# Performance work log

Hardware: AMD Instinct MI355X
Metric: run time of the kernel (lower is better)

## Reference

```python
import jax, jax.numpy as jnp
import numpy as np

B, S, E = 8, 1024, 512      # batch, seq, emb_size
L, H, K, F = 2, 4, 4, 128    # blocks, heads, conv kernel, final_size
I = 2 * E                    # inner dim (proj_factor=2)
DH = I // H                  # head dim
EPS = 1e-5


def _layernorm(x, g, b):
    mu = jnp.mean(x, axis=-1, keepdims=True)
    var = jnp.var(x, axis=-1, keepdims=True)
    return (x - mu) * jax.lax.rsqrt(var + EPS) * g + b


def _causal_conv(x, w, b):
    # x: [B,S,I], w: [K,I] depthwise, left-padded causal conv
    y = jax.lax.conv_general_dilated(
        x, w[:, None, :], window_strides=(1,), padding=[(K - 1, 0)],
        dimension_numbers=('NWC', 'WIO', 'NWC'), feature_group_count=I)
    return y + b


def _mlstm_parallel(q, k, v, ipre, fpre):
    # q,k,v: [B,H,S,DH]; ipre,fpre: [B,H,S]  (stabilized parallel mLSTM)
    lf = jax.nn.log_sigmoid(fpre)                       # [B,H,S]
    lfc = jnp.cumsum(lf, axis=-1)
    logD = lfc[..., :, None] - lfc[..., None, :] + ipre[..., None, :]  # [B,H,S,S]
    mask = jnp.tril(jnp.ones((S, S), dtype=bool))
    logD = jnp.where(mask, logD, -jnp.inf)
    m = jnp.max(logD, axis=-1, keepdims=True)           # [B,H,S,1]
    Dm = jnp.exp(logD - m)
    scores = jnp.einsum('bhtd,bhsd->bhts', q, k) * (DH ** -0.5) * Dm
    n = jnp.maximum(jnp.abs(jnp.sum(scores, axis=-1, keepdims=True)), jnp.exp(-m))
    return jnp.einsum('bhts,bhsd->bhtd', scores, v) / n


def _block(x, ln_g, ln_b, w_up, conv_w, conv_b, wq, wk, wv,
           w_i, b_i, w_f, b_f, skip, gn_g, w_down, b_down):
    res = x
    xn = _layernorm(x, ln_g, ln_b)
    up = xn @ w_up                                      # [B,S,2I]
    x_m, z = up[..., :I], up[..., I:]
    c_act = jax.nn.silu(_causal_conv(x_m, conv_w, conv_b))
    q = c_act @ wq
    k = c_act @ wk
    v = x_m @ wv
    qkv = jnp.concatenate([q, k, v], axis=-1)           # [B,S,3I]
    ipre = jnp.transpose(qkv @ w_i + b_i, (0, 2, 1))    # [B,H,S]
    fpre = jnp.transpose(qkv @ w_f + b_f, (0, 2, 1))
    to_h = lambda t: jnp.transpose(t.reshape(B, S, H, DH), (0, 2, 1, 3))
    h = _mlstm_parallel(to_h(q), to_h(k), to_h(v), ipre, fpre)  # [B,H,S,DH]
    # per-head group norm
    mu = jnp.mean(h, axis=-1, keepdims=True)
    var = jnp.var(h, axis=-1, keepdims=True)
    h = (h - mu) * jax.lax.rsqrt(var + EPS)
    h = jnp.transpose(h, (0, 2, 1, 3)).reshape(B, S, I) * gn_g
    h = h + skip * c_act
    h = h * jax.nn.silu(z)
    return res + h @ w_down + b_down


def setup_inputs() -> dict:
    key = jax.random.key(0)
    ks = jax.random.split(key, 12)
    n = lambda k, shp, s=0.02: jax.random.normal(k, shp, jnp.float32) * s
    return {
        'x': jax.random.normal(ks[0], (B, S, E), jnp.float32),
        'ln_g': jnp.ones((L, E), jnp.float32), 'ln_b': jnp.zeros((L, E), jnp.float32),
        'w_up': n(ks[1], (L, E, 2 * I)),
        'conv_w': n(ks[2], (L, K, I), 0.1), 'conv_b': jnp.zeros((L, I), jnp.float32),
        'wq': n(ks[3], (L, I, I)), 'wk': n(ks[4], (L, I, I)), 'wv': n(ks[5], (L, I, I)),
        'w_i': n(ks[6], (L, 3 * I, H)), 'b_i': jnp.zeros((L, H), jnp.float32),
        'w_f': n(ks[7], (L, 3 * I, H)), 'b_f': 3.0 * jnp.ones((L, H), jnp.float32),
        'skip': jnp.ones((L, I), jnp.float32), 'gn_g': jnp.ones((L, I), jnp.float32),
        'w_down': n(ks[8], (L, I, E)), 'b_down': jnp.zeros((L, E), jnp.float32),
        'w_fin': n(ks[9], (E, F)), 'b_fin': jnp.zeros((F,), jnp.float32),
    }


def reference(x, ln_g, ln_b, w_up, conv_w, conv_b, wq, wk, wv, w_i, b_i,
              w_f, b_f, skip, gn_g, w_down, b_down, w_fin, b_fin):
    h = x
    for l in range(L):  # 2 structurally identical mLSTM blocks
        h = _block(h, ln_g[l], ln_b[l], w_up[l], conv_w[l], conv_b[l],
                   wq[l], wk[l], wv[l], w_i[l], b_i[l], w_f[l], b_f[l],
                   skip[l], gn_g[l], w_down[l], b_down[l])
    return h @ w_fin + b_fin
```

## Files before the change

kernel.cpp:

```cpp
#include <hip/hip_runtime.h>
#include <math.h>

#define S_LEN 1024
#define I_DIM 1024
#define DH_   256
#define H_NUM 4
#define B_NUM 8
#define ROWS  (B_NUM*S_LEN)

#define GLOBAL_AS __attribute__((address_space(1)))
#define LDS_AS    __attribute__((address_space(3)))

#define VM0    asm volatile("s_waitcnt vmcnt(0)" ::: "memory")
#define LGKM0  asm volatile("s_waitcnt lgkmcnt(0)" ::: "memory")
#define BAR    __builtin_amdgcn_s_barrier()
#define SFENCE __builtin_amdgcn_sched_barrier(0)

typedef __attribute__((ext_vector_type(8))) short bf16x8;
typedef __attribute__((ext_vector_type(4))) float f32x4;
typedef unsigned short u16;

__device__ __forceinline__ u16 f2bf(float f) {
    union { float f; unsigned u; } v; v.f = f;
    unsigned r = v.u + 0x7FFF + ((v.u >> 16) & 1);
    return (u16)(r >> 16);
}
__device__ __forceinline__ float bf2f(u16 h) {
    union { unsigned u; float f; } v; v.u = ((unsigned)h) << 16;
    return v.f;
}

__global__ __launch_bounds__(64) void ln_fused_k(const float* __restrict__ x,
                                                 const float* __restrict__ g,
                                                 const float* __restrict__ b,
                                                 u16* __restrict__ out) {
    int row = blockIdx.x, lane = threadIdx.x;
    const float* xr = x + (size_t)row * 512;
    float4 a = *(const float4*)&xr[lane * 8];
    float4 c = *(const float4*)&xr[lane * 8 + 4];
    float s  = a.x + a.y + a.z + a.w + c.x + c.y + c.z + c.w;
    float s2 = a.x*a.x + a.y*a.y + a.z*a.z + a.w*a.w
             + c.x*c.x + c.y*c.y + c.z*c.z + c.w*c.w;
#pragma unroll
    for (int off = 32; off > 0; off >>= 1) {
        s  += __shfl_down(s, off);
        s2 += __shfl_down(s2, off);
    }
    s = __shfl(s, 0); s2 = __shfl(s2, 0);
    float mu = s * (1.f / 512.f);
    float rstd = rsqrtf(s2 * (1.f / 512.f) - mu * mu + 1e-5f);
    int e0 = lane * 8;
    float y[8] = {a.x,a.y,a.z,a.w,c.x,c.y,c.z,c.w};
    ushort4 o0, o1;
    o0.x = f2bf((y[0]-mu)*rstd*g[e0+0]+b[e0+0]);
    o0.y = f2bf((y[1]-mu)*rstd*g[e0+1]+b[e0+1]);
    o0.z = f2bf((y[2]-mu)*rstd*g[e0+2]+b[e0+2]);
    o0.w = f2bf((y[3]-mu)*rstd*g[e0+3]+b[e0+3]);
    o1.x = f2bf((y[4]-mu)*rstd*g[e0+4]+b[e0+4]);
    o1.y = f2bf((y[5]-mu)*rstd*g[e0+5]+b[e0+5]);
    o1.z = f2bf((y[6]-mu)*rstd*g[e0+6]+b[e0+6]);
    o1.w = f2bf((y[7]-mu)*rstd*g[e0+7]+b[e0+7]);
    *(ushort4*)&out[(size_t)row * 512 + e0]     = o0;
    *(ushort4*)&out[(size_t)row * 512 + e0 + 4] = o1;
}

__global__ __launch_bounds__(256) void cvtT_k(const float* __restrict__ W,
                                              u16* __restrict__ Wt, int K, int N) {
    __shared__ float t[32][33];
    int k0 = blockIdx.x * 32, n0 = blockIdx.y * 32;
    int c = threadIdx.x & 31, r8 = threadIdx.x >> 5;
#pragma unroll
    for (int q = 0; q < 4; q++) {
        int r = r8 * 4 + q;
        t[r][c] = W[(size_t)(k0 + r) * N + n0 + c];
    }
    __syncthreads();
#pragma unroll
    for (int q = 0; q < 4; q++) {
        int r = r8 * 4 + q;
        Wt[(size_t)(n0 + r) * K + k0 + c] = f2bf(t[c][r]);
    }
}

__global__ __launch_bounds__(256) void vt_k(const u16* __restrict__ v,
                                            u16* __restrict__ vt) {
    __shared__ u16 t[32][34];
    int s0 = blockIdx.x * 32, d0 = blockIdx.y * 32, bh = blockIdx.z;
    int b = bh >> 2, h = bh & 3;
    int c = threadIdx.x & 31, r4 = threadIdx.x >> 5;
#pragma unroll
    for (int q = 0; q < 4; q++) {
        int r = r4 * 4 + q;
        t[r][c] = v[(size_t)(b * 1024 + s0 + r) * I_DIM + h * 256 + d0 + c];
    }
    __syncthreads();
#pragma unroll
    for (int q = 0; q < 4; q++) {
        int r = r4 * 4 + q;
        vt[((size_t)bh * 256 + d0 + r) * 1024 + s0 + c] = t[c][r];
    }
}

template<int EPI>
__global__ __launch_bounds__(256) void gemm_bf16_k(
    const u16* __restrict__ A, const u16* __restrict__ Wt, int N, int K,
    float* __restrict__ Cf, u16* __restrict__ Cb,
    const float* __restrict__ bias, const float* __restrict__ res, int ldres)
{
    __shared__ __align__(16) u16 As[2][128 * 32];
    __shared__ __align__(16) u16 Bs[2][128 * 32];
    int tid = threadIdx.x;
    int lane = tid & 63;
    int wm = (tid >> 6) & 1, wn = tid >> 7;
    int gx = gridDim.x;
    int nwg = gx * gridDim.y;
    int bid = blockIdx.y * gx + blockIdx.x;
    int cpx = nwg >> 3;
    int swz = (bid & 7) * cpx + (bid >> 3);
    int r0 = (swz / gx) * 128, n0 = (swz % gx) * 128;

    int arow = tid >> 2, acol = (tid & 3) * 8;
    const u16* ap0 = A  + (size_t)(r0 + arow) * K + acol;
    const u16* ap1 = A  + (size_t)(r0 + 64 + arow) * K + acol;
    const u16* bp0 = Wt + (size_t)(n0 + arow) * K + acol;
    const u16* bp1 = Wt + (size_t)(n0 + 64 + arow) * K + acol;

    auto stage = [&](int kt, int bs) {
        int koff = kt * 32;
        __builtin_amdgcn_global_load_lds((const GLOBAL_AS unsigned int*)(ap0 + koff), (LDS_AS unsigned int*)&As[bs][tid * 8], 16, 0, 0);
        __builtin_amdgcn_global_load_lds((const GLOBAL_AS unsigned int*)(ap1 + koff), (LDS_AS unsigned int*)&As[bs][2048 + tid * 8], 16, 0, 0);
        __builtin_amdgcn_global_load_lds((const GLOBAL_AS unsigned int*)(bp0 + koff), (LDS_AS unsigned int*)&Bs[bs][tid * 8], 16, 0, 0);
        __builtin_amdgcn_global_load_lds((const GLOBAL_AS unsigned int*)(bp1 + koff), (LDS_AS unsigned int*)&Bs[bs][2048 + tid * 8], 16, 0, 0);
    };

    f32x4 acc[4][4];
#pragma unroll
    for (int i = 0; i < 4; i++)
#pragma unroll
        for (int j = 0; j < 4; j++) acc[i][j] = (f32x4){0.f, 0.f, 0.f, 0.f};

    int lm = lane & 15, lk = (lane >> 4) * 8;
    int nt = K >> 5;
    stage(0, 0);
    VM0; BAR; SFENCE;
    for (int t = 0; t < nt; ++t) {
        int cur = t & 1;
        if (t + 1 < nt) stage(t + 1, cur ^ 1);
        bf16x8 af[4], bfr[4];
#pragma unroll
        for (int f = 0; f < 4; f++) {
            af[f]  = *(const bf16x8*)&As[cur][(wm * 64 + f * 16 + lm) * 32 + lk];
            bfr[f] = *(const bf16x8*)&Bs[cur][(wn * 64 + f * 16 + lm) * 32 + lk];
        }
#pragma unroll
        for (int i = 0; i < 4; i++)
#pragma unroll
            for (int j = 0; j < 4; j++)
                acc[i][j] = __builtin_amdgcn_mfma_f32_16x16x32_bf16(af[i], bfr[j], acc[i][j], 0, 0, 0);
        VM0; BAR; SFENCE;
    }
    int lr = (lane >> 4) * 4;
#pragma unroll
    for (int i = 0; i < 4; i++) {
#pragma unroll
        for (int j = 0; j < 4; j++) {
#pragma unroll
            for (int q = 0; q < 4; q++) {
                int row = r0 + wm * 64 + i * 16 + lr + q;
                int col = n0 + wn * 64 + j * 16 + lm;
                float o = acc[i][j][q];
                if (EPI == 0) {
                    Cb[(size_t)row * N + col] = f2bf(o);
                } else if (EPI == 1) {
                    if (col < 1024) Cb[(size_t)row * 1024 + col] = f2bf(o);
                    else            Cf[(size_t)row * 1024 + (col - 1024)] = o;
                } else if (EPI == 2) {
                    o += bias[col] + res[(size_t)row * ldres + col];
                    Cf[(size_t)row * N + col] = o;
                    Cb[(size_t)row * N + col] = f2bf(o);
                } else {
                    o += bias[col];
                    Cf[(size_t)row * N + col] = o;
                }
            }
        }
    }
}

__global__ __launch_bounds__(256) void conv_k(const u16* __restrict__ xm,
                                              const float* __restrict__ w,
                                              const float* __restrict__ cb,
                                              u16* __restrict__ cact) {
    int idx = blockIdx.x * 256 + threadIdx.x;
    int r = idx >> 8;
    int c = (idx & 255) * 4;
    int t = r & 1023;
    const u16* base = xm + (size_t)(r - t) * I_DIM;
    float4 acc = *(const float4*)&cb[c];
#pragma unroll
    for (int j = 0; j < 4; j++) {
        int tt = t - 3 + j;
        if (tt >= 0) {
            short4 s = *(const short4*)&base[(size_t)tt * I_DIM + c];
            float4 wv = *(const float4*)&w[j * I_DIM + c];
            acc.x = fmaf(bf2f((u16)s.x), wv.x, acc.x);
            acc.y = fmaf(bf2f((u16)s.y), wv.y, acc.y);
            acc.z = fmaf(bf2f((u16)s.z), wv.z, acc.z);
            acc.w = fmaf(bf2f((u16)s.w), wv.w, acc.w);
        }
    }
    acc.x = acc.x / (1.f + __expf(-acc.x));
    acc.y = acc.y / (1.f + __expf(-acc.y));
    acc.z = acc.z / (1.f + __expf(-acc.z));
    acc.w = acc.w / (1.f + __expf(-acc.w));
    ushort4 o;
    o.x = f2bf(acc.x); o.y = f2bf(acc.y); o.z = f2bf(acc.z); o.w = f2bf(acc.w);
    *(ushort4*)&cact[(size_t)r * I_DIM + c] = o;
}

__global__ __launch_bounds__(256) void gates_k(const u16* __restrict__ qk,
                                               const u16* __restrict__ v,
                                               const float* __restrict__ wi,
                                               const float* __restrict__ bi,
                                               const float* __restrict__ wf,
                                               const float* __restrict__ bf,
                                               float* __restrict__ ipre,
                                               float* __restrict__ fpre) {
    int r0 = blockIdx.x * 4;
    int tid = threadIdx.x;
    float ai[4][4], af4[4][4];
#pragma unroll
    for (int r = 0; r < 4; r++)
#pragma unroll
        for (int m = 0; m < 4; m++) { ai[r][m] = 0.f; af4[r][m] = 0.f; }
#pragma unroll
    for (int part = 0; part < 3; part++) {
        const u16* src; size_t st;
        if (part == 0)      { src = qk + (size_t)r0 * 2048;        st = 2048; }
        else if (part == 1) { src = qk + (size_t)r0 * 2048 + 1024; st = 2048; }
        else                { src = v  + (size_t)r0 * 1024;        st = 1024; }
        const float* wip = wi + part * I_DIM * 4;
        const float* wfp = wf + part * I_DIM * 4;
#pragma unroll
        for (int jj = 0; jj < 4; jj++) {
            int e = tid + jj * 256;
            float4 w4  = *(const float4*)&wip[e * 4];
            float4 f4v = *(const float4*)&wfp[e * 4];
#pragma unroll
            for (int r = 0; r < 4; r++) {
                float xv = bf2f(src[(size_t)r * st + e]);
                ai[r][0] = fmaf(xv, w4.x, ai[r][0]);
                ai[r][1] = fmaf(xv, w4.y, ai[r][1]);
                ai[r][2] = fmaf(xv, w4.z, ai[r][2]);
                ai[r][3] = fmaf(xv, w4.w, ai[r][3]);
                af4[r][0] = fmaf(xv, f4v.x, af4[r][0]);
                af4[r][1] = fmaf(xv, f4v.y, af4[r][1]);
                af4[r][2] = fmaf(xv, f4v.z, af4[r][2]);
                af4[r][3] = fmaf(xv, f4v.w, af4[r][3]);
            }
        }
    }
#pragma unroll
    for (int off = 32; off > 0; off >>= 1) {
#pragma unroll
        for (int r = 0; r < 4; r++)
#pragma unroll
            for (int m = 0; m < 4; m++) {
                ai[r][m]  += __shfl_down(ai[r][m], off);
                af4[r][m] += __shfl_down(af4[r][m], off);
            }
    }
    __shared__ float red[4][32];
    int wv_ = tid >> 6, lane = tid & 63;
    if (lane == 0) {
#pragma unroll
        for (int r = 0; r < 4; r++)
#pragma unroll
            for (int m = 0; m < 4; m++) {
                red[wv_][r * 8 + m]     = ai[r][m];
                red[wv_][r * 8 + 4 + m] = af4[r][m];
            }
    }
    __syncthreads();
    if (tid < 32) {
        int r = tid >> 3, m = tid & 7;
        float s_ = red[0][tid] + red[1][tid] + red[2][tid] + red[3][tid];
        int row = r0 + r, bb = row >> 10, ss = row & 1023;
        if (m < 4) ipre[((size_t)(bb * 4 + m)) * 1024 + ss] = s_ + bi[m];
        else       fpre[((size_t)(bb * 4 + (m - 4))) * 1024 + ss] = s_ + bf[m - 4];
    }
}

__global__ __launch_bounds__(1024) void scan_k(const float* __restrict__ ipre,
                                               const float* __restrict__ fpre,
                                               float* __restrict__ cA,
                                               float* __restrict__ MA,
                                               float* __restrict__ nF) {
    __shared__ float buf[1024];
    int bh = blockIdx.x, t = threadIdx.x;
    size_t base = (size_t)bh * 1024;
    float fp = fpre[base + t];
    float lf = (fp >= 0.f) ? -log1pf(expf(-fp)) : (fp - log1pf(expf(fp)));
    buf[t] = lf; __syncthreads();
    for (int off = 1; off < 1024; off <<= 1) {
        float u = (t >= off) ? buf[t - off] : 0.f;
        __syncthreads();
        buf[t] += u;
        __syncthreads();
    }
    float lfc = buf[t];
    float c = ipre[base + t] - lfc;
    __syncthreads();
    buf[t] = c; __syncthreads();
    for (int off = 1; off < 1024; off <<= 1) {
        float u = (t >= off) ? buf[t - off] : -3.4e38f;
        __syncthreads();
        buf[t] = fmaxf(buf[t], u);
        __syncthreads();
    }
    float M = buf[t];
    cA[base + t] = c * 1.44269504f;
    MA[base + t] = M * 1.44269504f;
    nF[base + t] = expf(-(lfc + M));
}

__global__ __launch_bounds__(256) void attn_k(
    const u16* __restrict__ qg, const u16* __restrict__ kg, const u16* __restrict__ vt,
    const float* __restrict__ c2A, const float* __restrict__ M2A, const float* __restrict__ nFl,
    const u16* __restrict__ cact, const float* __restrict__ zb, u16* __restrict__ hb,
    const float* __restrict__ gng, const float* __restrict__ skip)
{
    __shared__ __align__(16) u16 Kb[2][32 * 256];
    __shared__ __align__(16) u16 Ps[32 * 40];
    __shared__ float rs2[4][16];
    __shared__ float rsI[32];
    __shared__ float gS[32 * 4];
    __shared__ float gQ[32 * 4];
    __shared__ float gmu[32], gvr[32];

    int tid = threadIdx.x;
    int w = tid >> 6, l = tid & 63;
    int lm = l & 15, lk = l >> 4;
    int i0 = blockIdx.x;
    int g = (i0 & 7) * 128 + (i0 >> 3);
    int b = g >> 7, h = (g >> 5) & 3, bx = g & 31;
    int T0 = (31 - bx) * 32;
    int tf = w & 1, sf = w >> 1;
    int bh32 = b * H_NUM + h;
    size_t bh = (size_t)bh32 * S_LEN;

    bf16x8 qf[8];
    {
        size_t base = ((size_t)(b * S_LEN + T0 + tf * 16 + lm)) * 2048 + h * DH_ + lk * 8;
#pragma unroll
        for (int ks = 0; ks < 8; ks++) qf[ks] = *(const bf16x8*)&qg[base + ks * 32];
    }
    f32x4 acc[2][4];
#pragma unroll
    for (int i = 0; i < 2; i++)
#pragma unroll
        for (int jd = 0; jd < 4; jd++) acc[i][jd] = (f32x4){0.f, 0.f, 0.f, 0.f};
    float rsum[4] = {0, 0, 0, 0};
    float m2r[4]; int tg[4];
#pragma unroll
    for (int q = 0; q < 4; q++) {
        tg[q] = T0 + tf * 16 + lk * 4 + q;
        m2r[q] = M2A[bh + tg[q]];
    }

    const size_t krow0 = (size_t)(b * S_LEN) * 2048 + h * DH_;
    const u16* vptr = vt + (size_t)bh32 * 256 * S_LEN + (size_t)(w * 64 + lm) * S_LEN + lk * 8;

    auto stageK = [&](int s0, int bs) {
#pragma unroll
        for (int r = 0; r < 4; r++) {
            int q = r * 256 + tid;
            int row = q >> 5, cl = q & 31;
            int cs = cl ^ (row & 7);
            const u16* src = kg + krow0 + (size_t)(s0 + row) * 2048 + cs * 8;
            __builtin_amdgcn_global_load_lds((const GLOBAL_AS unsigned int*)src,
                                             (LDS_AS unsigned int*)&Kb[bs][q * 8], 16, 0, 0);
        }
    };

    int nst = (T0 >> 5) + 1;
    stageK(0, 0);
    bf16x8 vA[4], vB[4];
    float c2c, c2n;
#pragma unroll
    for (int jd = 0; jd < 4; jd++) vA[jd] = *(const bf16x8*)(vptr + jd * 16 * S_LEN);
    c2c = c2A[bh + sf * 16 + lm];
    VM0; BAR; SFENCE;

    for (int st = 0; st < nst; st++) {
        int s0 = st * 32;
        int cur = st & 1;
        int more = (st + 1 < nst);
        if (more) {
            stageK(s0 + 32, cur ^ 1);
#pragma unroll
            for (int jd = 0; jd < 4; jd++) vB[jd] = *(const bf16x8*)(vptr + jd * 16 * S_LEN + s0 + 32);
            c2n = c2A[bh + s0 + 32 + sf * 16 + lm];
        }
        f32x4 sacc = (f32x4){0.f, 0.f, 0.f, 0.f};
        __builtin_amdgcn_s_setprio(1);
#pragma unroll
        for (int ks = 0; ks < 8; ks++) {
            int row = sf * 16 + lm;
            int ch = (ks * 4 + lk) ^ (row & 7);
            bf16x8 kf = *(const bf16x8*)&Kb[cur][row * 256 + ch * 8];
            sacc = __builtin_amdgcn_mfma_f32_16x16x32_bf16(qf[ks], kf, sacc, 0, 0, 0);
        }
        __builtin_amdgcn_s_setprio(0);
        {
            int sg = s0 + sf * 16 + lm;
#pragma unroll
            for (int q = 0; q < 4; q++) {
                float v = sacc[q] * 0.0625f * __builtin_amdgcn_exp2f(c2c - m2r[q]);
                v = (sg <= tg[q]) ? v : 0.f;
                u16 pb = f2bf(v);
                rsum[q] += bf2f(pb);
                Ps[(tf * 16 + lk * 4 + q) * 40 + sf * 16 + lm] = pb;
            }
        }
        LGKM0; BAR; SFENCE;
        __builtin_amdgcn_s_setprio(1);
#pragma unroll
        for (int i = 0; i < 2; i++) {
            bf16x8 pa = *(const bf16x8*)&Ps[(i * 16 + lm) * 40 + lk * 8];
#pragma unroll
            for (int jd = 0; jd < 4; jd++)
                acc[i][jd] = __builtin_amdgcn_mfma_f32_16x16x32_bf16(pa, vA[jd], acc[i][jd], 0, 0, 0);
        }
        __builtin_amdgcn_s_setprio(0);
        VM0; BAR; SFENCE;
        if (more) {
#pragma unroll
            for (int jd = 0; jd < 4; jd++) vA[jd] = vB[jd];
            c2c = c2n;
        }
    }
    {
#pragma unroll
        for (int m = 1; m < 16; m <<= 1) {
#pragma unroll
            for (int q = 0; q < 4; q++) rsum[q] += __shfl_xor(rsum[q], m);
        }
        if (lm == 0) {
#pragma unroll
            for (int q = 0; q < 4; q++) rs2[w][lk * 4 + q] = rsum[q];
        }
    }
    __syncthreads();
    if (tid < 32) {
        int tfi = tid >> 4, idx = tid & 15;
        float s = rs2[tfi][idx] + rs2[tfi + 2][idx];
        float n = fmaxf(fabsf(s), nFl[bh + T0 + tid]);
        rsI[tid] = 1.f / n;
    }
    __syncthreads();
#pragma unroll
    for (int i = 0; i < 2; i++) {
#pragma unroll
        for (int q = 0; q < 4; q++) {
            int rl = i * 16 + lk * 4 + q;
            float inv = rsI[rl];
            float ps = 0.f, pq = 0.f;
#pragma unroll
            for (int jd = 0; jd < 4; jd++) {
                float v = acc[i][jd][q] * inv;
                acc[i][jd][q] = v;
                ps += v; pq += v * v;
            }
#pragma unroll
            for (int m = 1; m < 16; m <<= 1) {
                ps += __shfl_xor(ps, m);
                pq += __shfl_xor(pq, m);
            }
            if (lm == 0) { gS[rl * 4 + w] = ps; gQ[rl * 4 + w] = pq; }
        }
    }
    __syncthreads();
    if (tid < 32) {
        float s1 = gS[tid*4] + gS[tid*4+1] + gS[tid*4+2] + gS[tid*4+3];
        float s2 = gQ[tid*4] + gQ[tid*4+1] + gQ[tid*4+2] + gQ[tid*4+3];
        float mu = s1 * (1.f / 256.f);
        float var = s2 * (1.f / 256.f) - mu * mu;
        gmu[tid] = mu;
        gvr[tid] = rsqrtf(var + 1e-5f);
    }
    __syncthreads();
#pragma unroll
    for (int i = 0; i < 2; i++) {
#pragma unroll
        for (int q = 0; q < 4; q++) {
            int rl = i * 16 + lk * 4 + q;
            size_t r = (size_t)b * S_LEN + T0 + rl;
            float mu = gmu[rl], rv = gvr[rl];
#pragma unroll
            for (int jd = 0; jd < 4; jd++) {
                int cix = h * DH_ + w * 64 + jd * 16 + lm;
                float val = (acc[i][jd][q] - mu) * rv * gng[cix];
                float ca = bf2f(cact[r * I_DIM + cix]);
                float z = zb[r * I_DIM + cix];
                float hm = (val + skip[cix] * ca) * (z / (1.f + __expf(-z)));
                hb[r * I_DIM + cix] = f2bf(hm);
            }
        }
    }
}

extern "C" void kernel_launch(void* const* d_in, const int* in_sizes, int n_in,
                              void* d_out, int out_size, void* d_ws, size_t ws_size,
                              hipStream_t stream) {
    const float* x      = (const float*)d_in[0];
    const float* ln_g   = (const float*)d_in[1];
    const float* ln_b   = (const float*)d_in[2];
    const float* w_up   = (const float*)d_in[3];
    const float* conv_w = (const float*)d_in[4];
    const float* conv_b = (const float*)d_in[5];
    const float* wq     = (const float*)d_in[6];
    const float* wk     = (const float*)d_in[7];
    const float* wv     = (const float*)d_in[8];
    const float* w_i    = (const float*)d_in[9];
    const float* b_i    = (const float*)d_in[10];
    const float* w_f    = (const float*)d_in[11];
    const float* b_f    = (const float*)d_in[12];
    const float* skip   = (const float*)d_in[13];
    const float* gn_g   = (const float*)d_in[14];
    const float* w_down = (const float*)d_in[15];
    const float* b_down = (const float*)d_in[16];
    const float* w_fin  = (const float*)d_in[17];
    const float* b_fin  = (const float*)d_in[18];

    char* p = (char*)d_ws;
    auto alloc = [&](size_t bytes) { void* r = p; p += (bytes + 255) & ~(size_t)255; return r; };
    float* zbuf  = (float*)alloc((size_t)ROWS * 1024 * 4);
    float* xa    = (float*)alloc((size_t)ROWS * 512 * 4);
    float* xb2   = (float*)alloc((size_t)ROWS * 512 * 4);
    u16*  xln    = (u16*)alloc((size_t)ROWS * 512 * 2);
    u16*  xm     = (u16*)alloc((size_t)ROWS * 1024 * 2);
    u16*  cactb  = (u16*)alloc((size_t)ROWS * 1024 * 2);
    u16*  qkbf   = (u16*)alloc((size_t)ROWS * 2048 * 2);
    u16*  vbf    = (u16*)alloc((size_t)ROWS * 1024 * 2);
    u16*  vtg    = (u16*)alloc((size_t)32 * 256 * 1024 * 2);
    u16*  hbf    = (u16*)alloc((size_t)ROWS * 1024 * 2);
    u16*  xoutb  = (u16*)alloc((size_t)ROWS * 512 * 2);
    u16*  wupT   = (u16*)alloc((size_t)2 * 2048 * 512 * 2);
    u16*  wqkT   = (u16*)alloc((size_t)2 * 2048 * 1024 * 2);
    u16*  wvT    = (u16*)alloc((size_t)2 * 1024 * 1024 * 2);
    u16*  wdT    = (u16*)alloc((size_t)2 * 512 * 1024 * 2);
    u16*  wfT    = (u16*)alloc((size_t)128 * 512 * 2);
    float* ipre  = (float*)alloc(32768 * 4);
    float* fpre  = (float*)alloc(32768 * 4);
    float* cA    = (float*)alloc(32768 * 4);
    float* MA    = (float*)alloc(32768 * 4);
    float* nF    = (float*)alloc(32768 * 4);

    for (int l = 0; l < 2; l++) {
        cvtT_k<<<dim3(16, 64), 256, 0, stream>>>(w_up + (size_t)l * 512 * 2048, wupT + (size_t)l * 2048 * 512, 512, 2048);
        cvtT_k<<<dim3(32, 32), 256, 0, stream>>>(wq + (size_t)l * 1024 * 1024, wqkT + (size_t)l * 2048 * 1024, 1024, 1024);
        cvtT_k<<<dim3(32, 32), 256, 0, stream>>>(wk + (size_t)l * 1024 * 1024, wqkT + (size_t)l * 2048 * 1024 + 1024 * 1024, 1024, 1024);
        cvtT_k<<<dim3(32, 32), 256, 0, stream>>>(wv + (size_t)l * 1024 * 1024, wvT + (size_t)l * 1024 * 1024, 1024, 1024);
        cvtT_k<<<dim3(32, 16), 256, 0, stream>>>(w_down + (size_t)l * 1024 * 512, wdT + (size_t)l * 512 * 1024, 1024, 512);
    }
    cvtT_k<<<dim3(16, 4), 256, 0, stream>>>(w_fin, wfT, 512, 128);

    const float* xin = x;
    for (int l = 0; l < 2; l++) {
        float* xout = (l == 0) ? xa : xb2;
        ln_fused_k<<<ROWS, 64, 0, stream>>>(xin, ln_g + l * 512, ln_b + l * 512, xln);
        gemm_bf16_k<1><<<dim3(16, 64), 256, 0, stream>>>(
            xln, wupT + (size_t)l * 2048 * 512, 2048, 512, zbuf, xm, nullptr, nullptr, 0);
        conv_k<<<ROWS, 256, 0, stream>>>(xm, conv_w + l * 4 * I_DIM, conv_b + l * I_DIM, cactb);
        gemm_bf16_k<0><<<dim3(8, 64), 256, 0, stream>>>(
            xm, wvT + (size_t)l * 1024 * 1024, 1024, 1024, nullptr, vbf, nullptr, nullptr, 0);
        gemm_bf16_k<0><<<dim3(16, 64), 256, 0, stream>>>(
            cactb, wqkT + (size_t)l * 2048 * 1024, 2048, 1024, nullptr, qkbf, nullptr, nullptr, 0);
        vt_k<<<dim3(32, 8, 32), 256, 0, stream>>>(vbf, vtg);
        gates_k<<<ROWS / 4, 256, 0, stream>>>(qkbf, vbf,
            w_i + l * 3072 * 4, b_i + l * 4, w_f + l * 3072 * 4, b_f + l * 4, ipre, fpre);
        scan_k<<<32, 1024, 0, stream>>>(ipre, fpre, cA, MA, nF);
        attn_k<<<dim3(1024), 256, 0, stream>>>(qkbf, qkbf + 1024, vtg, cA, MA, nF, cactb, zbuf, hbf,
            gn_g + l * I_DIM, skip + l * I_DIM);
        gemm_bf16_k<2><<<dim3(4, 64), 256, 0, stream>>>(
            hbf, wdT + (size_t)l * 512 * 1024, 512, 1024, xout, xoutb,
            b_down + l * 512, xin, 512);
        xin = xout;
    }
    gemm_bf16_k<3><<<dim3(1, 64), 256, 0, stream>>>(
        xoutb, wfT, 128, 512, (float*)d_out, nullptr, b_fin, nullptr, 0);
}
```

Baseline: 714.9 us.

## Software-pipeline attention loop so QK of step t overlaps PV of step t-1

Restructures the causal attention loop so the score MFMAs for the current K tile run alongside the PV MFMAs for the previous tile. The P tile is double-buffered in LDS, and the per-iteration barrier count drops from two to one, removing the explicit vmcnt wait. V fragments are now loaded one step later, into a staging register set. The gain is fewer barriers and more independent MFMA work per iteration. The risk is that the asynchronous LDS K loads are no longer guaranteed complete before the barrier, which depends on how the compiler places the vmcnt wait.

```diff
diff --git a/kernel.cpp b/kernel.cpp
--- a/kernel.cpp
+++ b/kernel.cpp
@@ -331,7 +331,7 @@
     const float* __restrict__ gng, const float* __restrict__ skip)
 {
     __shared__ __align__(16) u16 Kb[2][32 * 256];
-    __shared__ __align__(16) u16 Ps[32 * 40];
+    __shared__ __align__(16) u16 Ps[2][32 * 40];
     __shared__ float rs2[4][16];
     __shared__ float rsI[32];
     __shared__ float gS[32 * 4];
@@ -387,32 +387,30 @@
     stageK(0, 0);
     bf16x8 vA[4], vB[4];
     float c2c, c2n;
-#pragma unroll
-    for (int jd = 0; jd < 4; jd++) vA[jd] = *(const bf16x8*)(vptr + jd * 16 * S_LEN);
     c2c = c2A[bh + sf * 16 + lm];
     VM0; BAR; SFENCE;
 
-    for (int st = 0; st < nst; st++) {
-        int s0 = st * 32;
-        int cur = st & 1;
-        int more = (st + 1 < nst);
-        if (more) {
-            stageK(s0 + 32, cur ^ 1);
-#pragma unroll
-            for (int jd = 0; jd < 4; jd++) vB[jd] = *(const bf16x8*)(vptr + jd * 16 * S_LEN + s0 + 32);
-            c2n = c2A[bh + s0 + 32 + sf * 16 + lm];
-        }
-        f32x4 sacc = (f32x4){0.f, 0.f, 0.f, 0.f};
-        __builtin_amdgcn_s_setprio(1);
-#pragma unroll
-        for (int ks = 0; ks < 8; ks++) {
-            int row = sf * 16 + lm;
-            int ch = (ks * 4 + lk) ^ (row & 7);
-            bf16x8 kf = *(const bf16x8*)&Kb[cur][row * 256 + ch * 8];
-            sacc = __builtin_amdgcn_mfma_f32_16x16x32_bf16(qf[ks], kf, sacc, 0, 0, 0);
-        }
-        __builtin_amdgcn_s_setprio(0);
-        {
+    for (int t = 0; t <= nst; t++) {
+        int s0 = t * 32;
+        int kc = t & 1;
+        bool qp = (t < nst);
+        bool more = (t + 1 < nst);
+        if (qp) {
+            if (more) stageK(s0 + 32, kc ^ 1);
+            SFENCE;
+#pragma unroll
+            for (int jd = 0; jd < 4; jd++) vB[jd] = *(const bf16x8*)(vptr + jd * 16 * S_LEN + s0);
+            if (more) c2n = c2A[bh + s0 + 32 + sf * 16 + lm];
+            f32x4 sacc = (f32x4){0.f, 0.f, 0.f, 0.f};
+            __builtin_amdgcn_s_setprio(1);
+#pragma unroll
+            for (int ks = 0; ks < 8; ks++) {
+                int row = sf * 16 + lm;
+                int ch = (ks * 4 + lk) ^ (row & 7);
+                bf16x8 kf = *(const bf16x8*)&Kb[kc][row * 256 + ch * 8];
+                sacc = __builtin_amdgcn_mfma_f32_16x16x32_bf16(qf[ks], kf, sacc, 0, 0, 0);
+            }
+            __builtin_amdgcn_s_setprio(0);
             int sg = s0 + sf * 16 + lm;
 #pragma unroll
             for (int q = 0; q < 4; q++) {
@@ -420,25 +418,26 @@
                 v = (sg <= tg[q]) ? v : 0.f;
                 u16 pb = f2bf(v);
                 rsum[q] += bf2f(pb);
-                Ps[(tf * 16 + lk * 4 + q) * 40 + sf * 16 + lm] = pb;
-            }
+                Ps[kc][(tf * 16 + lk * 4 + q) * 40 + sf * 16 + lm] = pb;
+            }
+        }
+        if (t > 0) {
+            __builtin_amdgcn_s_setprio(1);
+#pragma unroll
+            for (int i = 0; i < 2; i++) {
+                bf16x8 pa = *(const bf16x8*)&Ps[kc ^ 1][(i * 16 + lm) * 40 + lk * 8];
+#pragma unroll
+                for (int jd = 0; jd < 4; jd++)
+                    acc[i][jd] = __builtin_amdgcn_mfma_f32_16x16x32_bf16(pa, vA[jd], acc[i][jd], 0, 0, 0);
+            }
+            __builtin_amdgcn_s_setprio(0);
+        }
+        if (qp) {
+#pragma unroll
+            for (int jd = 0; jd < 4; jd++) vA[jd] = vB[jd];
+            if (more) c2c = c2n;
         }
         LGKM0; BAR; SFENCE;
-        __builtin_amdgcn_s_setprio(1);
-#pragma unroll
-        for (int i = 0; i < 2; i++) {
-            bf16x8 pa = *(const bf16x8*)&Ps[(i * 16 + lm) * 40 + lk * 8];
-#pragma unroll
-            for (int jd = 0; jd < 4; jd++)
-                acc[i][jd] = __builtin_amdgcn_mfma_f32_16x16x32_bf16(pa, vA[jd], acc[i][jd], 0, 0, 0);
-        }
-        __builtin_amdgcn_s_setprio(0);
-        VM0; BAR; SFENCE;
-        if (more) {
-#pragma unroll
-            for (int jd = 0; jd < 4; jd++) vA[jd] = vB[jd];
-            c2c = c2n;
-        }
     }
     {
 #pragma unroll
```

Measured after the change: 712.3 us. About the same (-0.4%).

## Give each wave its own 16-row query tile in mLSTM attention, dropping LDS staging

Applied to the files above, without the earlier changes.

Restructures the attention kernel so each wave independently owns a 16-row query tile over the full 256-wide head dimension. K and V fragments are now loaded straight from global memory instead of being staged cooperatively into double-buffered LDS. Block-wide barriers are gone, and the normalisation and group-norm reductions now happen within a wave via shuffles. The grid is halved and the launch bound now requests 3 blocks per CU. In exchange, K/V reuse across waves through LDS is lost, there is no prefetch overlap, and register pressure rises from 16 accumulator tiles per wave.

```diff
diff --git a/kernel.cpp b/kernel.cpp
--- a/kernel.cpp
+++ b/kernel.cpp
@@ -324,188 +324,127 @@
     nF[base + t] = expf(-(lfc + M));
 }
 
-__global__ __launch_bounds__(256) void attn_k(
+__global__ __launch_bounds__(256, 3) void attn_k(
     const u16* __restrict__ qg, const u16* __restrict__ kg, const u16* __restrict__ vt,
     const float* __restrict__ c2A, const float* __restrict__ M2A, const float* __restrict__ nFl,
     const u16* __restrict__ cact, const float* __restrict__ zb, u16* __restrict__ hb,
     const float* __restrict__ gng, const float* __restrict__ skip)
 {
-    __shared__ __align__(16) u16 Kb[2][32 * 256];
-    __shared__ __align__(16) u16 Ps[32 * 40];
-    __shared__ float rs2[4][16];
-    __shared__ float rsI[32];
-    __shared__ float gS[32 * 4];
-    __shared__ float gQ[32 * 4];
-    __shared__ float gmu[32], gvr[32];
+    __shared__ __align__(16) u16 Ps[4][16 * 40];
 
     int tid = threadIdx.x;
     int w = tid >> 6, l = tid & 63;
     int lm = l & 15, lk = l >> 4;
-    int i0 = blockIdx.x;
-    int g = (i0 & 7) * 128 + (i0 >> 3);
-    int b = g >> 7, h = (g >> 5) & 3, bx = g & 31;
-    int T0 = (31 - bx) * 32;
-    int tf = w & 1, sf = w >> 1;
+    int bid = blockIdx.x;
+    int g = (bid & 7) * 64 + (bid >> 3);
+    int b = g >> 6, rr = g & 63;
+    int h = rr >> 4, tb = rr & 15;
+    int tt = tb * 4 + w;
+    int T0w = (63 - tt) * 16;
+    int nst = (T0w >> 5) + 1;
     int bh32 = b * H_NUM + h;
     size_t bh = (size_t)bh32 * S_LEN;
 
     bf16x8 qf[8];
     {
-        size_t base = ((size_t)(b * S_LEN + T0 + tf * 16 + lm)) * 2048 + h * DH_ + lk * 8;
-#pragma unroll
-        for (int ks = 0; ks < 8; ks++) qf[ks] = *(const bf16x8*)&qg[base + ks * 32];
-    }
-    f32x4 acc[2][4];
-#pragma unroll
-    for (int i = 0; i < 2; i++)
-#pragma unroll
-        for (int jd = 0; jd < 4; jd++) acc[i][jd] = (f32x4){0.f, 0.f, 0.f, 0.f};
+        size_t qbase = ((size_t)(b * S_LEN + T0w + lm)) * 2048 + h * DH_ + lk * 8;
+#pragma unroll
+        for (int ks = 0; ks < 8; ks++) qf[ks] = *(const bf16x8*)&qg[qbase + ks * 32];
+    }
+    f32x4 acc[16];
+#pragma unroll
+    for (int jd = 0; jd < 16; jd++) acc[jd] = (f32x4){0.f, 0.f, 0.f, 0.f};
     float rsum[4] = {0, 0, 0, 0};
     float m2r[4]; int tg[4];
 #pragma unroll
     for (int q = 0; q < 4; q++) {
-        tg[q] = T0 + tf * 16 + lk * 4 + q;
+        tg[q] = T0w + lk * 4 + q;
         m2r[q] = M2A[bh + tg[q]];
     }
 
-    const size_t krow0 = (size_t)(b * S_LEN) * 2048 + h * DH_;
-    const u16* vptr = vt + (size_t)bh32 * 256 * S_LEN + (size_t)(w * 64 + lm) * S_LEN + lk * 8;
-
-    auto stageK = [&](int s0, int bs) {
-#pragma unroll
-        for (int r = 0; r < 4; r++) {
-            int q = r * 256 + tid;
-            int row = q >> 5, cl = q & 31;
-            int cs = cl ^ (row & 7);
-            const u16* src = kg + krow0 + (size_t)(s0 + row) * 2048 + cs * 8;
-            __builtin_amdgcn_global_load_lds((const GLOBAL_AS unsigned int*)src,
-                                             (LDS_AS unsigned int*)&Kb[bs][q * 8], 16, 0, 0);
-        }
-    };
-
-    int nst = (T0 >> 5) + 1;
-    stageK(0, 0);
-    bf16x8 vA[4], vB[4];
-    float c2c, c2n;
-#pragma unroll
-    for (int jd = 0; jd < 4; jd++) vA[jd] = *(const bf16x8*)(vptr + jd * 16 * S_LEN);
-    c2c = c2A[bh + sf * 16 + lm];
-    VM0; BAR; SFENCE;
+    const u16* kp0 = kg + (size_t)(b * S_LEN + lm) * 2048 + h * DH_ + lk * 8;
+    const u16* kp1 = kp0 + 16 * 2048;
+    const u16* vp  = vt + ((size_t)bh32 * 256 + lm) * S_LEN + lk * 8;
+    u16* Pw = Ps[w];
 
     for (int st = 0; st < nst; st++) {
         int s0 = st * 32;
-        int cur = st & 1;
-        int more = (st + 1 < nst);
-        if (more) {
-            stageK(s0 + 32, cur ^ 1);
-#pragma unroll
-            for (int jd = 0; jd < 4; jd++) vB[jd] = *(const bf16x8*)(vptr + jd * 16 * S_LEN + s0 + 32);
-            c2n = c2A[bh + s0 + 32 + sf * 16 + lm];
-        }
-        f32x4 sacc = (f32x4){0.f, 0.f, 0.f, 0.f};
-        __builtin_amdgcn_s_setprio(1);
+        float c2x0 = c2A[bh + s0 + lm];
+        float c2x1 = c2A[bh + s0 + 16 + lm];
+        f32x4 sa0 = (f32x4){0.f,0.f,0.f,0.f};
+        f32x4 sa1 = (f32x4){0.f,0.f,0.f,0.f};
+        const u16* k0p = kp0 + (size_t)s0 * 2048;
+        const u16* k1p = kp1 + (size_t)s0 * 2048;
 #pragma unroll
         for (int ks = 0; ks < 8; ks++) {
-            int row = sf * 16 + lm;
-            int ch = (ks * 4 + lk) ^ (row & 7);
-            bf16x8 kf = *(const bf16x8*)&Kb[cur][row * 256 + ch * 8];
-            sacc = __builtin_amdgcn_mfma_f32_16x16x32_bf16(qf[ks], kf, sacc, 0, 0, 0);
-        }
-        __builtin_amdgcn_s_setprio(0);
-        {
-            int sg = s0 + sf * 16 + lm;
+            bf16x8 k0 = *(const bf16x8*)(k0p + ks * 32);
+            bf16x8 k1 = *(const bf16x8*)(k1p + ks * 32);
+            sa0 = __builtin_amdgcn_mfma_f32_16x16x32_bf16(qf[ks], k0, sa0, 0, 0, 0);
+            sa1 = __builtin_amdgcn_mfma_f32_16x16x32_bf16(qf[ks], k1, sa1, 0, 0, 0);
+        }
+#pragma unroll
+        for (int js = 0; js < 2; js++) {
+            int sg = s0 + js * 16 + lm;
+            float c2 = js ? c2x1 : c2x0;
 #pragma unroll
             for (int q = 0; q < 4; q++) {
-                float v = sacc[q] * 0.0625f * __builtin_amdgcn_exp2f(c2c - m2r[q]);
+                float v = (js ? sa1[q] : sa0[q]) * 0.0625f * __builtin_amdgcn_exp2f(c2 - m2r[q]);
                 v = (sg <= tg[q]) ? v : 0.f;
                 u16 pb = f2bf(v);
                 rsum[q] += bf2f(pb);
-                Ps[(tf * 16 + lk * 4 + q) * 40 + sf * 16 + lm] = pb;
+                Pw[(lk * 4 + q) * 40 + js * 16 + lm] = pb;
             }
         }
-        LGKM0; BAR; SFENCE;
-        __builtin_amdgcn_s_setprio(1);
-#pragma unroll
-        for (int i = 0; i < 2; i++) {
-            bf16x8 pa = *(const bf16x8*)&Ps[(i * 16 + lm) * 40 + lk * 8];
-#pragma unroll
-            for (int jd = 0; jd < 4; jd++)
-                acc[i][jd] = __builtin_amdgcn_mfma_f32_16x16x32_bf16(pa, vA[jd], acc[i][jd], 0, 0, 0);
-        }
-        __builtin_amdgcn_s_setprio(0);
-        VM0; BAR; SFENCE;
-        if (more) {
-#pragma unroll
-            for (int jd = 0; jd < 4; jd++) vA[jd] = vB[jd];
-            c2c = c2n;
-        }
-    }
-    {
+        SFENCE; LGKM0; SFENCE;
+        bf16x8 pa = *(const bf16x8*)&Pw[lm * 40 + lk * 8];
+        const u16* vsp = vp + s0;
+#pragma unroll
+        for (int jd = 0; jd < 16; jd++) {
+            bf16x8 vf = *(const bf16x8*)(vsp + (size_t)jd * 16 * S_LEN);
+            acc[jd] = __builtin_amdgcn_mfma_f32_16x16x32_bf16(pa, vf, acc[jd], 0, 0, 0);
+        }
+        SFENCE;
+    }
+#pragma unroll
+    for (int m = 1; m < 16; m <<= 1) {
+#pragma unroll
+        for (int q = 0; q < 4; q++) rsum[q] += __shfl_xor(rsum[q], m);
+    }
+    float inv[4];
+#pragma unroll
+    for (int q = 0; q < 4; q++) {
+        float n = fmaxf(fabsf(rsum[q]), nFl[bh + tg[q]]);
+        inv[q] = 1.f / n;
+    }
+    float mu[4], rstd[4];
+#pragma unroll
+    for (int q = 0; q < 4; q++) {
+        float ps = 0.f, pq = 0.f;
+#pragma unroll
+        for (int jd = 0; jd < 16; jd++) {
+            float v = acc[jd][q] * inv[q];
+            acc[jd][q] = v;
+            ps += v; pq += v * v;
+        }
 #pragma unroll
         for (int m = 1; m < 16; m <<= 1) {
-#pragma unroll
-            for (int q = 0; q < 4; q++) rsum[q] += __shfl_xor(rsum[q], m);
-        }
-        if (lm == 0) {
-#pragma unroll
-            for (int q = 0; q < 4; q++) rs2[w][lk * 4 + q] = rsum[q];
-        }
-    }
-    __syncthreads();
-    if (tid < 32) {
-        int tfi = tid >> 4, idx = tid & 15;
-        float s = rs2[tfi][idx] + rs2[tfi + 2][idx];
-        float n = fmaxf(fabsf(s), nFl[bh + T0 + tid]);
-        rsI[tid] = 1.f / n;
-    }
-    __syncthreads();
-#pragma unroll
-    for (int i = 0; i < 2; i++) {
-#pragma unroll
-        for (int q = 0; q < 4; q++) {
-            int rl = i * 16 + lk * 4 + q;
-            float inv = rsI[rl];
-            float ps = 0.f, pq = 0.f;
-#pragma unroll
-            for (int jd = 0; jd < 4; jd++) {
-                float v = acc[i][jd][q] * inv;
-                acc[i][jd][q] = v;
-                ps += v; pq += v * v;
-            }
-#pragma unroll
-            for (int m = 1; m < 16; m <<= 1) {
-                ps += __shfl_xor(ps, m);
-                pq += __shfl_xor(pq, m);
-            }
-            if (lm == 0) { gS[rl * 4 + w] = ps; gQ[rl * 4 + w] = pq; }
-        }
-    }
-    __syncthreads();
-    if (tid < 32) {
-        float s1 = gS[tid*4] + gS[tid*4+1] + gS[tid*4+2] + gS[tid*4+3];
-        float s2 = gQ[tid*4] + gQ[tid*4+1] + gQ[tid*4+2] + gQ[tid*4+3];
-        float mu = s1 * (1.f / 256.f);
-        float var = s2 * (1.f / 256.f) - mu * mu;
-        gmu[tid] = mu;
-        gvr[tid] = rsqrtf(var + 1e-5f);
-    }
-    __syncthreads();
-#pragma unroll
-    for (int i = 0; i < 2; i++) {
-#pragma unroll
-        for (int q = 0; q < 4; q++) {
-            int rl = i * 16 + lk * 4 + q;
-            size_t r = (size_t)b * S_LEN + T0 + rl;
-            float mu = gmu[rl], rv = gvr[rl];
-#pragma unroll
-            for (int jd = 0; jd < 4; jd++) {
-                int cix = h * DH_ + w * 64 + jd * 16 + lm;
-                float val = (acc[i][jd][q] - mu) * rv * gng[cix];
-                float ca = bf2f(cact[r * I_DIM + cix]);
-                float z = zb[r * I_DIM + cix];
-                float hm = (val + skip[cix] * ca) * (z / (1.f + __expf(-z)));
-                hb[r * I_DIM + cix] = f2bf(hm);
-            }
+            ps += __shfl_xor(ps, m);
+            pq += __shfl_xor(pq, m);
+        }
+        mu[q] = ps * (1.f / 256.f);
+        rstd[q] = rsqrtf(pq * (1.f / 256.f) - mu[q] * mu[q] + 1e-5f);
+    }
+#pragma unroll
+    for (int q = 0; q < 4; q++) {
+        size_t r = (size_t)b * S_LEN + tg[q];
+#pragma unroll
+        for (int jd = 0; jd < 16; jd++) {
+            int cix = h * DH_ + jd * 16 + lm;
+            float val = (acc[jd][q] - mu[q]) * rstd[q] * gng[cix];
+            float ca = bf2f(cact[r * I_DIM + cix]);
+            float z = zb[r * I_DIM + cix];
+            float hm = (val + skip[cix] * ca) * (z / (1.f + __expf(-z)));
+            hb[r * I_DIM + cix] = f2bf(hm);
         }
     }
 }
@@ -581,7 +520,7 @@
         gates_k<<<ROWS / 4, 256, 0, stream>>>(qkbf, vbf,
             w_i + l * 3072 * 4, b_i + l * 4, w_f + l * 3072 * 4, b_f + l * 4, ipre, fpre);
         scan_k<<<32, 1024, 0, stream>>>(ipre, fpre, cA, MA, nF);
-        attn_k<<<dim3(1024), 256, 0, stream>>>(qkbf, qkbf + 1024, vtg, cA, MA, nF, cactb, zbuf, hbf,
+        attn_k<<<dim3(512), 256, 0, stream>>>(qkbf, qkbf + 1024, vtg, cA, MA, nF, cactb, zbuf, hbf,
             gn_g + l * I_DIM, skip + l * I_DIM);
         gemm_bf16_k<2><<<dim3(4, 64), 256, 0, stream>>>(
             hbf, wdT + (size_t)l * 512 * 1024, 512, 1024, xout, xoutb,
```

New measurement: 994.8 us. +39.2%, slower.
